# Kernel optimization log

Measured on AMD Instinct MI355X. Metric: run time of the kernel, lower is better.

The kernel has to match this reference:

```python
import jax, jax.numpy as jnp
import numpy as np

N_NODES = 50000


def _gcn_conv(x, src, dst, W, b, num_nodes):
    """PyG GCNConv: out = D^{-1/2}(A+I)D^{-1/2} (x @ W) + b, self-loops added."""
    h = x @ W  # [N, out]
    # degrees over edges incl. self-loops (src/dst already include self-loops)
    ones = jnp.ones(src.shape[0], dtype=h.dtype)
    deg = jax.ops.segment_sum(ones, dst, num_segments=num_nodes)
    dinv = jnp.where(deg > 0, jax.lax.rsqrt(deg), 0.0)
    norm = dinv[src] * dinv[dst]  # [E]
    msgs = h[src] * norm[:, None]  # [E, out] gather (memory-bound)
    out = jax.ops.segment_sum(msgs, dst, num_segments=num_nodes)
    return out + b


def setup_inputs() -> dict:
    key = jax.random.key(0)
    ks = jax.random.split(key, 8)
    in_c, h2, h1, out_c = 256, 256, 128, 128
    x = jax.random.normal(ks[0], (N_NODES, in_c), dtype=jnp.float32)
    edge_index = jax.random.randint(ks[1], (2, 800000), 0, N_NODES, dtype=jnp.int64)
    def glorot(k, fi, fo):
        s = float(np.sqrt(6.0 / (fi + fo)))
        return jax.random.uniform(k, (fi, fo), jnp.float32, -s, s)
    return {
        "x": x,
        "edge_index": edge_index,
        "W1": glorot(ks[2], in_c, h2), "b1": jnp.zeros((h2,), jnp.float32),
        "W2": glorot(ks[3], h2, h1), "b2": jnp.zeros((h1,), jnp.float32),
        "W3": glorot(ks[4], h1, out_c), "b3": jnp.zeros((out_c,), jnp.float32),
    }


def reference(x, edge_index, W1, b1, W2, b2, W3, b3):
    n = x.shape[0]
    loops = jnp.arange(n, dtype=edge_index.dtype)
    src = jnp.concatenate([edge_index[0], loops])
    dst = jnp.concatenate([edge_index[1], loops])
    # dropout is a no-op in eval mode (training=False)
    h1 = jax.nn.relu(_gcn_conv(x, src, dst, W1, b1, n))
    h2 = jax.nn.relu(_gcn_conv(h1, src, dst, W2, b2, n))
    h3 = jax.nn.relu(_gcn_conv(h2, src, dst, W3, b3, n))
    return jnp.concatenate([h1, h2, h3], axis=1)
```

## Files before the change

### kernel.cpp

```cpp
#include <hip/hip_runtime.h>

typedef __attribute__((ext_vector_type(8))) short bfrag8;
typedef __attribute__((ext_vector_type(4))) float f32x4v;

__device__ inline short f2bf(float f) {
    unsigned u = __builtin_bit_cast(unsigned, f);
    u = (u + 0x7FFFu + ((u >> 16) & 1u)) >> 16;
    return (short)u;
}
__device__ inline float bf2f(short s) {
    unsigned u = ((unsigned)(unsigned short)s) << 16;
    return __builtin_bit_cast(float, u);
}
__device__ inline int pack2(short lo, short hi) {
    return (int)(((unsigned)(unsigned short)lo) | (((unsigned)(unsigned short)hi) << 16));
}


__global__ void deg_count_kernel(const int* __restrict__ dst, int E, int* __restrict__ deg) {
    int e = blockIdx.x * blockDim.x + threadIdx.x;
    if (e < E) atomicAdd(&deg[dst[e]], 1);
}

__global__ void block_sum_kernel(const int* __restrict__ deg, int n, int* __restrict__ bsums) {
    int i = blockIdx.x * 256 + threadIdx.x;
    int v = (i < n) ? deg[i] : 0;
#pragma unroll
    for (int off = 32; off > 0; off >>= 1) v += __shfl_down(v, off);
    __shared__ int wsum[4];
    int lane = threadIdx.x & 63, w = threadIdx.x >> 6;
    if (lane == 0) wsum[w] = v;
    __syncthreads();
    if (threadIdx.x == 0) bsums[blockIdx.x] = wsum[0] + wsum[1] + wsum[2] + wsum[3];
}

__global__ void scan_bsums_kernel(int* __restrict__ bsums, int B, int* __restrict__ offs, int n) {
    __shared__ int s[256];
    int tid = threadIdx.x;
    int v = (tid < B) ? bsums[tid] : 0;
    s[tid] = v;
    __syncthreads();
    for (int off = 1; off < 256; off <<= 1) {
        int t = (tid >= off) ? s[tid - off] : 0;
        __syncthreads();
        s[tid] += t;
        __syncthreads();
    }
    if (tid < B) bsums[tid] = (tid == 0) ? 0 : s[tid - 1];
    if (tid == 0) offs[n] = s[255];
}

__global__ void scan_final_kernel(const int* __restrict__ deg, int n,
                                  const int* __restrict__ bsums,
                                  int* __restrict__ offs, int* __restrict__ cursor,
                                  float* __restrict__ dinv) {
    __shared__ int s[256];
    int tid = threadIdx.x;
    int i = blockIdx.x * 256 + tid;
    int v = (i < n) ? deg[i] : 0;
    s[tid] = v;
    __syncthreads();
    for (int off = 1; off < 256; off <<= 1) {
        int t = (tid >= off) ? s[tid - off] : 0;
        __syncthreads();
        s[tid] += t;
        __syncthreads();
    }
    if (i < n) {
        int excl = s[tid] - v + bsums[blockIdx.x];
        offs[i] = excl;
        cursor[i] = excl;
        dinv[i] = rsqrtf((float)(v + 1));
    }
}

__global__ void csr_fill_kernel(const int* __restrict__ src, const int* __restrict__ dst, int E,
                                int* __restrict__ cursor, int* __restrict__ csr) {
    int e = blockIdx.x * blockDim.x + threadIdx.x;
    if (e < E) {
        int d = dst[e];
        int p = atomicAdd(&cursor[d], 1);
        csr[p] = src[e];
    }
}


__global__ void wt_kernel(const float* __restrict__ W, short* __restrict__ Wt,
                          int K, int logN) {
    int i = blockIdx.x * blockDim.x + threadIdx.x;
    int total = K << logN;
    if (i < total) {
        int k = i >> logN;
        int n = i & ((1 << logN) - 1);
        Wt[(size_t)n * K + k] = f2bf(W[i]);
    }
}


#define ALD 40

__global__ __launch_bounds__(256) void gemm_mfma_kernel(
        const float* __restrict__ A, int lda,
        const short* __restrict__ Bt, int K,
        const float* __restrict__ dinv,
        short* __restrict__ Tout, int ldt,
        int M) {
    __shared__ short As[128][ALD];
    __shared__ short Bs[128][ALD];

    const int tid = threadIdx.x;
    const int lane = tid & 63;
    const int wid = tid >> 6;
    const int l15 = lane & 15;
    const int quad = lane >> 4;
    const int q8 = quad * 8;
    const int bm = blockIdx.x * 128;
    const int bn = blockIdx.y * 128;
    const int wm = (wid & 1) * 64;
    const int wn = (wid >> 1) * 64;

    f32x4v acc[4][4];
#pragma unroll
    for (int i = 0; i < 4; ++i)
#pragma unroll
        for (int j = 0; j < 4; ++j) acc[i][j] = (f32x4v){0.f, 0.f, 0.f, 0.f};

    const int srow = tid >> 1;
    const int sseg = (tid & 1) * 16;

    for (int k0 = 0; k0 < K; k0 += 32) {
        {
            int grow = bm + srow;
            float4 v0 = {0,0,0,0}, v1 = {0,0,0,0}, v2 = {0,0,0,0}, v3 = {0,0,0,0};
            if (grow < M) {
                const float* p = A + (size_t)grow * lda + k0 + sseg;
                v0 = *(const float4*)(p + 0);
                v1 = *(const float4*)(p + 4);
                v2 = *(const float4*)(p + 8);
                v3 = *(const float4*)(p + 12);
            }
            int4 w0 = make_int4(pack2(f2bf(v0.x), f2bf(v0.y)), pack2(f2bf(v0.z), f2bf(v0.w)),
                                pack2(f2bf(v1.x), f2bf(v1.y)), pack2(f2bf(v1.z), f2bf(v1.w)));
            int4 w1 = make_int4(pack2(f2bf(v2.x), f2bf(v2.y)), pack2(f2bf(v2.z), f2bf(v2.w)),
                                pack2(f2bf(v3.x), f2bf(v3.y)), pack2(f2bf(v3.z), f2bf(v3.w)));
            *(int4*)&As[srow][sseg] = w0;
            *(int4*)&As[srow][sseg + 8] = w1;
        }
        {
            const short* p = Bt + (size_t)(bn + srow) * K + k0 + sseg;
            int4 w0 = *(const int4*)p;
            int4 w1 = *(const int4*)(p + 8);
            *(int4*)&Bs[srow][sseg] = w0;
            *(int4*)&Bs[srow][sseg + 8] = w1;
        }
        __syncthreads();

        bfrag8 af[4], bfv[4];
#pragma unroll
        for (int mt = 0; mt < 4; ++mt)
            af[mt] = *(const bfrag8*)&As[wm + mt * 16 + l15][q8];
#pragma unroll
        for (int nt = 0; nt < 4; ++nt)
            bfv[nt] = *(const bfrag8*)&Bs[wn + nt * 16 + l15][q8];
#pragma unroll
        for (int mt = 0; mt < 4; ++mt)
#pragma unroll
            for (int nt = 0; nt < 4; ++nt)
                acc[mt][nt] = __builtin_amdgcn_mfma_f32_16x16x32_bf16(af[mt], bfv[nt], acc[mt][nt], 0, 0, 0);
        __syncthreads();
    }

#pragma unroll
    for (int mt = 0; mt < 4; ++mt) {
#pragma unroll
        for (int r = 0; r < 4; ++r) {
            int grow = bm + wm + mt * 16 + quad * 4 + r;
            if (grow < M) {
                float di = dinv[grow];
                short* outp = Tout + (size_t)grow * ldt + bn + wn + l15;
#pragma unroll
                for (int nt = 0; nt < 4; ++nt)
                    outp[nt * 16] = f2bf(acc[mt][nt][r] * di);
            }
        }
    }
}


template<int C>
__global__ __launch_bounds__(256) void agg_kernel(
        const short* __restrict__ hn, const float* __restrict__ dinv,
        const int* __restrict__ offs, const int* __restrict__ csr,
        const float* __restrict__ bias, float* __restrict__ out,
        int coloff, int n) {
    constexpr int V = C / 64;
    int node = blockIdx.x * 4 + (threadIdx.x >> 6);
    if (node >= n) return;
    int lane = threadIdx.x & 63;
    const short* base = hn + lane * V;

    float acc[V];
#pragma unroll
    for (int v = 0; v < V; ++v) acc[v] = 0.f;

    int beg = offs[node], end = offs[node + 1];
    int e = beg;
    if (V == 4) {
        for (; e + 4 <= end; e += 4) {
            int s0 = csr[e], s1 = csr[e + 1], s2 = csr[e + 2], s3 = csr[e + 3];
            short4 a = *(const short4*)(base + (size_t)s0 * C);
            short4 b = *(const short4*)(base + (size_t)s1 * C);
            short4 c = *(const short4*)(base + (size_t)s2 * C);
            short4 d = *(const short4*)(base + (size_t)s3 * C);
            acc[0] += bf2f(a.x) + bf2f(b.x) + bf2f(c.x) + bf2f(d.x);
            acc[1] += bf2f(a.y) + bf2f(b.y) + bf2f(c.y) + bf2f(d.y);
            acc[2] += bf2f(a.z) + bf2f(b.z) + bf2f(c.z) + bf2f(d.z);
            acc[3] += bf2f(a.w) + bf2f(b.w) + bf2f(c.w) + bf2f(d.w);
        }
        for (; e < end; ++e) {
            short4 a = *(const short4*)(base + (size_t)csr[e] * C);
            acc[0] += bf2f(a.x); acc[1] += bf2f(a.y); acc[2] += bf2f(a.z); acc[3] += bf2f(a.w);
        }
        short4 a = *(const short4*)(base + (size_t)node * C);
        acc[0] += bf2f(a.x); acc[1] += bf2f(a.y); acc[2] += bf2f(a.z); acc[3] += bf2f(a.w);
    } else {
        for (; e + 4 <= end; e += 4) {
            int s0 = csr[e], s1 = csr[e + 1], s2 = csr[e + 2], s3 = csr[e + 3];
            short2 a = *(const short2*)(base + (size_t)s0 * C);
            short2 b = *(const short2*)(base + (size_t)s1 * C);
            short2 c = *(const short2*)(base + (size_t)s2 * C);
            short2 d = *(const short2*)(base + (size_t)s3 * C);
            acc[0] += bf2f(a.x) + bf2f(b.x) + bf2f(c.x) + bf2f(d.x);
            acc[1] += bf2f(a.y) + bf2f(b.y) + bf2f(c.y) + bf2f(d.y);
        }
        for (; e < end; ++e) {
            short2 a = *(const short2*)(base + (size_t)csr[e] * C);
            acc[0] += bf2f(a.x); acc[1] += bf2f(a.y);
        }
        short2 a = *(const short2*)(base + (size_t)node * C);
        acc[0] += bf2f(a.x); acc[1] += bf2f(a.y);
    }

    float di = dinv[node];
    float* op = out + (size_t)node * 512 + coloff + lane * V;
    if (V == 4) {
        float4 o;
        o.x = fmaxf(fmaf(di, acc[0], bias[lane * 4 + 0]), 0.f);
        o.y = fmaxf(fmaf(di, acc[1], bias[lane * 4 + 1]), 0.f);
        o.z = fmaxf(fmaf(di, acc[2], bias[lane * 4 + 2]), 0.f);
        o.w = fmaxf(fmaf(di, acc[3], bias[lane * 4 + 3]), 0.f);
        *(float4*)op = o;
    } else {
        float2 o;
        o.x = fmaxf(fmaf(di, acc[0], bias[lane * 2 + 0]), 0.f);
        o.y = fmaxf(fmaf(di, acc[1], bias[lane * 2 + 1]), 0.f);
        *(float2*)op = o;
    }
}


extern "C" void kernel_launch(void* const* d_in, const int* in_sizes, int n_in,
                              void* d_out, int out_size, void* d_ws, size_t ws_size,
                              hipStream_t stream) {
    const float* x  = (const float*)d_in[0];
    const int*   ei = (const int*)d_in[1];
    const float* W1 = (const float*)d_in[2];
    const float* b1 = (const float*)d_in[3];
    const float* W2 = (const float*)d_in[4];
    const float* b2 = (const float*)d_in[5];
    const float* W3 = (const float*)d_in[6];
    const float* b3 = (const float*)d_in[7];

    const int IN_C = 256, H2 = 256, H1 = 128, OUT_C = 128;
    int n = in_sizes[0] / IN_C;
    int E = in_sizes[1] / 2;
    const int* src = ei;
    const int* dst = ei + E;

    char* ws = (char*)d_ws;
    auto carve = [&](size_t bytes) { char* p = ws; ws += (bytes + 255) & ~(size_t)255; return p; };
    int*   deg    = (int*)  carve((size_t)n * 4);
    int*   offs   = (int*)  carve(((size_t)n + 1) * 4);
    int*   cursor = (int*)  carve((size_t)n * 4);
    float* dinv   = (float*)carve((size_t)n * 4);
    int*   csr    = (int*)  carve((size_t)E * 4);
    int*   bsums  = (int*)  carve(256 * 4);
    short* Wt1    = (short*)carve((size_t)IN_C * H2 * 2);
    short* Wt2    = (short*)carve((size_t)H2 * H1 * 2);
    short* Wt3    = (short*)carve((size_t)H1 * OUT_C * 2);
    short* t      = (short*)carve((size_t)n * 256 * 2);

    float* out = (float*)d_out;

    int nblk = (n + 255) / 256;

    hipMemsetAsync(deg, 0, (size_t)n * sizeof(int), stream);
    deg_count_kernel<<<(E + 255) / 256, 256, 0, stream>>>(dst, E, deg);
    block_sum_kernel<<<nblk, 256, 0, stream>>>(deg, n, bsums);
    scan_bsums_kernel<<<1, 256, 0, stream>>>(bsums, nblk, offs, n);
    scan_final_kernel<<<nblk, 256, 0, stream>>>(deg, n, bsums, offs, cursor, dinv);
    csr_fill_kernel<<<(E + 255) / 256, 256, 0, stream>>>(src, dst, E, cursor, csr);

    wt_kernel<<<(IN_C * H2 + 255) / 256, 256, 0, stream>>>(W1, Wt1, IN_C, 8);
    wt_kernel<<<(H2 * H1 + 255) / 256, 256, 0, stream>>>(W2, Wt2, H2, 7);
    wt_kernel<<<(H1 * OUT_C + 255) / 256, 256, 0, stream>>>(W3, Wt3, H1, 7);

    int mb = (n + 127) / 128;

    gemm_mfma_kernel<<<dim3(mb, H2 / 128), 256, 0, stream>>>(x, IN_C, Wt1, IN_C, dinv, t, H2, n);
    agg_kernel<256><<<(n + 3) / 4, 256, 0, stream>>>(t, dinv, offs, csr, b1, out, 0, n);

    gemm_mfma_kernel<<<dim3(mb, H1 / 128), 256, 0, stream>>>(out, 512, Wt2, H2, dinv, t, H1, n);
    agg_kernel<128><<<(n + 3) / 4, 256, 0, stream>>>(t, dinv, offs, csr, b2, out, H2, n);

    gemm_mfma_kernel<<<dim3(mb, OUT_C / 128), 256, 0, stream>>>(out + H2, 512, Wt3, H1, dinv, t, OUT_C, n);
    agg_kernel<128><<<(n + 3) / 4, 256, 0, stream>>>(t, dinv, offs, csr, b3, out, H2 + H1, n);
}
```

Before: 431.5 us.

## Stage bf16 GEMM inputs via direct global-to-LDS loads and deeper gather unroll

Converts x to bf16 in a separate pass and has each aggregation kernel also write a bf16 copy of its activations, so the following GEMM reads half-size bf16 inputs. The GEMM now loads A and B tiles straight into LDS with global_load_lds, dropping the register staging and fp32-to-bf16 conversion inside the main loop. The LDS tiles lose their padding, which may cause bank conflicts. The aggregation gather loop is unrolled to 8 edges to keep more loads in flight. The costs are an extra conversion pass, extra bf16 writes, a larger workspace, and no bounds guard on rows past n, which is handled by padding the buffers to a multiple of 128 rows.

```diff
diff --git a/kernel.cpp b/kernel.cpp
--- a/kernel.cpp
+++ b/kernel.cpp
@@ -14,6 +14,11 @@
 }
 __device__ inline int pack2(short lo, short hi) {
     return (int)(((unsigned)(unsigned short)lo) | (((unsigned)(unsigned short)hi) << 16));
+}
+__device__ inline void gload_lds16(const short* g, short* l) {
+    __builtin_amdgcn_global_load_lds(
+        (const __attribute__((address_space(1))) void*)g,
+        (__attribute__((address_space(3))) void*)l, 16, 0, 0);
 }
 
 
@@ -97,16 +102,26 @@
 }
 
 
-#define ALD 40
-
-__global__ __launch_bounds__(256) void gemm_mfma_kernel(
-        const float* __restrict__ A, int lda,
+__global__ void x2b_kernel(const float* __restrict__ x, short* __restrict__ xb, int total8) {
+    int i = blockIdx.x * blockDim.x + threadIdx.x;
+    if (i < total8) {
+        const float4* p = (const float4*)(x + (size_t)i * 8);
+        float4 v0 = p[0], v1 = p[1];
+        int4 w = make_int4(pack2(f2bf(v0.x), f2bf(v0.y)), pack2(f2bf(v0.z), f2bf(v0.w)),
+                           pack2(f2bf(v1.x), f2bf(v1.y)), pack2(f2bf(v1.z), f2bf(v1.w)));
+        *(int4*)(xb + (size_t)i * 8) = w;
+    }
+}
+
+
+__global__ __launch_bounds__(256) void gemm_bf16_kernel(
+        const short* __restrict__ A, int lda,
         const short* __restrict__ Bt, int K,
         const float* __restrict__ dinv,
         short* __restrict__ Tout, int ldt,
         int M) {
-    __shared__ short As[128][ALD];
-    __shared__ short Bs[128][ALD];
+    __shared__ short As[128 * 32];
+    __shared__ short Bs[128 * 32];
 
     const int tid = threadIdx.x;
     const int lane = tid & 63;
@@ -125,43 +140,32 @@
 #pragma unroll
         for (int j = 0; j < 4; ++j) acc[i][j] = (f32x4v){0.f, 0.f, 0.f, 0.f};
 
-    const int srow = tid >> 1;
-    const int sseg = (tid & 1) * 16;
+    const int f0 = wid * 2048 + lane * 16;
+    const int r0 = f0 >> 6, c0 = (f0 & 63) >> 1;
+    const int f1 = f0 + 1024;
+    const int r1 = f1 >> 6, c1 = (f1 & 63) >> 1;
+    short* ldsA = As + wid * 1024;
+    short* ldsB = Bs + wid * 1024;
+
+    const short* a0 = A + (size_t)(bm + r0) * lda + c0;
+    const short* a1 = A + (size_t)(bm + r1) * lda + c1;
+    const short* b0 = Bt + (size_t)(bn + r0) * K + c0;
+    const short* b1 = Bt + (size_t)(bn + r1) * K + c1;
 
     for (int k0 = 0; k0 < K; k0 += 32) {
-        {
-            int grow = bm + srow;
-            float4 v0 = {0,0,0,0}, v1 = {0,0,0,0}, v2 = {0,0,0,0}, v3 = {0,0,0,0};
-            if (grow < M) {
-                const float* p = A + (size_t)grow * lda + k0 + sseg;
-                v0 = *(const float4*)(p + 0);
-                v1 = *(const float4*)(p + 4);
-                v2 = *(const float4*)(p + 8);
-                v3 = *(const float4*)(p + 12);
-            }
-            int4 w0 = make_int4(pack2(f2bf(v0.x), f2bf(v0.y)), pack2(f2bf(v0.z), f2bf(v0.w)),
-                                pack2(f2bf(v1.x), f2bf(v1.y)), pack2(f2bf(v1.z), f2bf(v1.w)));
-            int4 w1 = make_int4(pack2(f2bf(v2.x), f2bf(v2.y)), pack2(f2bf(v2.z), f2bf(v2.w)),
-                                pack2(f2bf(v3.x), f2bf(v3.y)), pack2(f2bf(v3.z), f2bf(v3.w)));
-            *(int4*)&As[srow][sseg] = w0;
-            *(int4*)&As[srow][sseg + 8] = w1;
-        }
-        {
-            const short* p = Bt + (size_t)(bn + srow) * K + k0 + sseg;
-            int4 w0 = *(const int4*)p;
-            int4 w1 = *(const int4*)(p + 8);
-            *(int4*)&Bs[srow][sseg] = w0;
-            *(int4*)&Bs[srow][sseg + 8] = w1;
-        }
+        gload_lds16(a0 + k0, ldsA);
+        gload_lds16(a1 + k0, ldsA + 512);
+        gload_lds16(b0 + k0, ldsB);
+        gload_lds16(b1 + k0, ldsB + 512);
         __syncthreads();
 
         bfrag8 af[4], bfv[4];
 #pragma unroll
         for (int mt = 0; mt < 4; ++mt)
-            af[mt] = *(const bfrag8*)&As[wm + mt * 16 + l15][q8];
+            af[mt] = *(const bfrag8*)&As[(wm + mt * 16 + l15) * 32 + q8];
 #pragma unroll
         for (int nt = 0; nt < 4; ++nt)
-            bfv[nt] = *(const bfrag8*)&Bs[wn + nt * 16 + l15][q8];
+            bfv[nt] = *(const bfrag8*)&Bs[(wn + nt * 16 + l15) * 32 + q8];
 #pragma unroll
         for (int mt = 0; mt < 4; ++mt)
 #pragma unroll
@@ -187,12 +191,12 @@
 }
 
 
-template<int C>
+template<int C, bool WB>
 __global__ __launch_bounds__(256) void agg_kernel(
         const short* __restrict__ hn, const float* __restrict__ dinv,
         const int* __restrict__ offs, const int* __restrict__ csr,
         const float* __restrict__ bias, float* __restrict__ out,
-        int coloff, int n) {
+        short* __restrict__ hb, int coloff, int n) {
     constexpr int V = C / 64;
     int node = blockIdx.x * 4 + (threadIdx.x >> 6);
     if (node >= n) return;
@@ -206,16 +210,16 @@
     int beg = offs[node], end = offs[node + 1];
     int e = beg;
     if (V == 4) {
-        for (; e + 4 <= end; e += 4) {
-            int s0 = csr[e], s1 = csr[e + 1], s2 = csr[e + 2], s3 = csr[e + 3];
-            short4 a = *(const short4*)(base + (size_t)s0 * C);
-            short4 b = *(const short4*)(base + (size_t)s1 * C);
-            short4 c = *(const short4*)(base + (size_t)s2 * C);
-            short4 d = *(const short4*)(base + (size_t)s3 * C);
-            acc[0] += bf2f(a.x) + bf2f(b.x) + bf2f(c.x) + bf2f(d.x);
-            acc[1] += bf2f(a.y) + bf2f(b.y) + bf2f(c.y) + bf2f(d.y);
-            acc[2] += bf2f(a.z) + bf2f(b.z) + bf2f(c.z) + bf2f(d.z);
-            acc[3] += bf2f(a.w) + bf2f(b.w) + bf2f(c.w) + bf2f(d.w);
+        for (; e + 8 <= end; e += 8) {
+            short4 r[8];
+#pragma unroll
+            for (int j = 0; j < 8; ++j)
+                r[j] = *(const short4*)(base + (size_t)csr[e + j] * C);
+#pragma unroll
+            for (int j = 0; j < 8; ++j) {
+                acc[0] += bf2f(r[j].x); acc[1] += bf2f(r[j].y);
+                acc[2] += bf2f(r[j].z); acc[3] += bf2f(r[j].w);
+            }
         }
         for (; e < end; ++e) {
             short4 a = *(const short4*)(base + (size_t)csr[e] * C);
@@ -224,14 +228,15 @@
         short4 a = *(const short4*)(base + (size_t)node * C);
         acc[0] += bf2f(a.x); acc[1] += bf2f(a.y); acc[2] += bf2f(a.z); acc[3] += bf2f(a.w);
     } else {
-        for (; e + 4 <= end; e += 4) {
-            int s0 = csr[e], s1 = csr[e + 1], s2 = csr[e + 2], s3 = csr[e + 3];
-            short2 a = *(const short2*)(base + (size_t)s0 * C);
-            short2 b = *(const short2*)(base + (size_t)s1 * C);
-            short2 c = *(const short2*)(base + (size_t)s2 * C);
-            short2 d = *(const short2*)(base + (size_t)s3 * C);
-            acc[0] += bf2f(a.x) + bf2f(b.x) + bf2f(c.x) + bf2f(d.x);
-            acc[1] += bf2f(a.y) + bf2f(b.y) + bf2f(c.y) + bf2f(d.y);
+        for (; e + 8 <= end; e += 8) {
+            short2 r[8];
+#pragma unroll
+            for (int j = 0; j < 8; ++j)
+                r[j] = *(const short2*)(base + (size_t)csr[e + j] * C);
+#pragma unroll
+            for (int j = 0; j < 8; ++j) {
+                acc[0] += bf2f(r[j].x); acc[1] += bf2f(r[j].y);
+            }
         }
         for (; e < end; ++e) {
             short2 a = *(const short2*)(base + (size_t)csr[e] * C);
@@ -242,19 +247,23 @@
     }
 
     float di = dinv[node];
+    float res[V];
+#pragma unroll
+    for (int v = 0; v < V; ++v)
+        res[v] = fmaxf(fmaf(di, acc[v], bias[lane * V + v]), 0.f);
+
     float* op = out + (size_t)node * 512 + coloff + lane * V;
     if (V == 4) {
-        float4 o;
-        o.x = fmaxf(fmaf(di, acc[0], bias[lane * 4 + 0]), 0.f);
-        o.y = fmaxf(fmaf(di, acc[1], bias[lane * 4 + 1]), 0.f);
-        o.z = fmaxf(fmaf(di, acc[2], bias[lane * 4 + 2]), 0.f);
-        o.w = fmaxf(fmaf(di, acc[3], bias[lane * 4 + 3]), 0.f);
-        *(float4*)op = o;
+        *(float4*)op = make_float4(res[0], res[1], res[2], res[3]);
+        if (WB) {
+            int2 w = make_int2(pack2(f2bf(res[0]), f2bf(res[1])), pack2(f2bf(res[2]), f2bf(res[3])));
+            *(int2*)(hb + (size_t)node * C + lane * V) = w;
+        }
     } else {
-        float2 o;
-        o.x = fmaxf(fmaf(di, acc[0], bias[lane * 2 + 0]), 0.f);
-        o.y = fmaxf(fmaf(di, acc[1], bias[lane * 2 + 1]), 0.f);
-        *(float2*)op = o;
+        *(float2*)op = make_float2(res[0], res[1]);
+        if (WB) {
+            *(int*)(hb + (size_t)node * C + lane * V) = pack2(f2bf(res[0]), f2bf(res[1]));
+        }
     }
 }
 
@@ -277,6 +286,9 @@
     const int* src = ei;
     const int* dst = ei + E;
 
+    int mb = (n + 127) / 128;
+    int npad = mb * 128;
+
     char* ws = (char*)d_ws;
     auto carve = [&](size_t bytes) { char* p = ws; ws += (bytes + 255) & ~(size_t)255; return p; };
     int*   deg    = (int*)  carve((size_t)n * 4);
@@ -288,10 +300,10 @@
     short* Wt1    = (short*)carve((size_t)IN_C * H2 * 2);
     short* Wt2    = (short*)carve((size_t)H2 * H1 * 2);
     short* Wt3    = (short*)carve((size_t)H1 * OUT_C * 2);
-    short* t      = (short*)carve((size_t)n * 256 * 2);
+    short* t      = (short*)carve((size_t)npad * 256 * 2);
+    short* inb    = (short*)carve((size_t)npad * 256 * 2);
 
     float* out = (float*)d_out;
-
     int nblk = (n + 255) / 256;
 
     hipMemsetAsync(deg, 0, (size_t)n * sizeof(int), stream);
@@ -305,14 +317,15 @@
     wt_kernel<<<(H2 * H1 + 255) / 256, 256, 0, stream>>>(W2, Wt2, H2, 7);
     wt_kernel<<<(H1 * OUT_C + 255) / 256, 256, 0, stream>>>(W3, Wt3, H1, 7);
 
-    int mb = (n + 127) / 128;
-
-    gemm_mfma_kernel<<<dim3(mb, H2 / 128), 256, 0, stream>>>(x, IN_C, Wt1, IN_C, dinv, t, H2, n);
-    agg_kernel<256><<<(n + 3) / 4, 256, 0, stream>>>(t, dinv, offs, csr, b1, out, 0, n);
-
-    gemm_mfma_kernel<<<dim3(mb, H1 / 128), 256, 0, stream>>>(out, 512, Wt2, H2, dinv, t, H1, n);
-    agg_kernel<128><<<(n + 3) / 4, 256, 0, stream>>>(t, dinv, offs, csr, b2, out, H2, n);
-
-    gemm_mfma_kernel<<<dim3(mb, OUT_C / 128), 256, 0, stream>>>(out + H2, 512, Wt3, H1, dinv, t, OUT_C, n);
-    agg_kernel<128><<<(n + 3) / 4, 256, 0, stream>>>(t, dinv, offs, csr, b3, out, H2 + H1, n);
-}
+    int total8 = n * IN_C / 8;
+    x2b_kernel<<<(total8 + 255) / 256, 256, 0, stream>>>(x, inb, total8);
+
+    gemm_bf16_kernel<<<dim3(mb, H2 / 128), 256, 0, stream>>>(inb, IN_C, Wt1, IN_C, dinv, t, H2, n);
+    agg_kernel<256, true><<<(n + 3) / 4, 256, 0, stream>>>(t, dinv, offs, csr, b1, out, inb, 0, n);
+
+    gemm_bf16_kernel<<<dim3(mb, H1 / 128), 256, 0, stream>>>(inb, H2, Wt2, H2, dinv, t, H1, n);
+    agg_kernel<128, true><<<(n + 3) / 4, 256, 0, stream>>>(t, dinv, offs, csr, b2, out, inb, H2, n);
+
+    gemm_bf16_kernel<<<dim3(mb, OUT_C / 128), 256, 0, stream>>>(inb, H1, Wt3, H1, dinv, t, OUT_C, n);
+    agg_kernel<128, false><<<(n + 3) / 4, 256, 0, stream>>>(t, dinv, offs, csr, b3, out, nullptr, H2 + H1, n);
+}
```

After: 445.2 us. 3.2% more time.
